# Performance work log

Hardware: AMD Instinct MI355X
Metric: run time of the kernel (lower is better)

The kernel has to match this reference:

```python
import jax, jax.numpy as jnp
import numpy as np

TAU_MEM = 20.0          # tau for both ExpLeak (syn) and LIF (mem)
SPIKE_THRESHOLD = 1.0
WIDTH_GRAD = 0.5        # surrogate gradient width (unused in fwd)
SCALE_GRAD = 1.0


def setup_inputs() -> dict:
    key = jax.random.key(0)
    k1, k2 = jax.random.split(key)
    x = jax.random.normal(k1, (32, 2048, 512, 1), dtype=jnp.float32)
    weight = jax.random.uniform(k2, (1, 1), dtype=jnp.float32)  # Linear(1,1,bias=False) weight (set to scalar `weight` in torch)
    return {"x": x, "weight": weight}


def reference(x, weight):
    # x: (B, T, N, 1); weight: (1, 1)
    alpha = jnp.exp(jnp.asarray(-1.0 / TAU_MEM, dtype=x.dtype))
    i_in = x * weight[0, 0]                      # Linear(1,1,no bias)
    i_in = jnp.moveaxis(i_in, 1, 0)              # (T, B, N, 1) for scan over time

    def step(carry, i_t):
        v_syn, v_mem = carry
        # ExpLeak, norm_input=False: v_syn = alpha*v_syn + input
        v_syn = alpha * v_syn + i_t
        # LIF, norm_input=False: decay then integrate synaptic current
        v_mem = alpha * v_mem + v_syn
        # SingleSpike: at most one spike per step
        spk = (v_mem >= SPIKE_THRESHOLD).astype(v_mem.dtype)
        # MembraneSubtract reset
        v_mem = v_mem - SPIKE_THRESHOLD * spk
        return (v_syn, v_mem), spk

    zeros = jnp.zeros_like(i_in[0])
    _, spikes = jax.lax.scan(step, (zeros, zeros), i_in)
    return jnp.moveaxis(spikes, 0, 1)            # (B, T, N, 1)
```

## Files before the change

### kernel.cpp

```cpp
#include <hip/hip_runtime.h>
#include <math.h>


constexpr int T_ = 2048;
constexpr int N_ = 512;
constexpr int TILE = 64;
constexpr int NTILE = T_ / TILE;
constexpr int NCH = 64;
constexpr int NBUF = 4;

typedef const __attribute__((address_space(1))) void* gas_ptr;
typedef __attribute__((address_space(3))) void* las_ptr;

__global__ __launch_bounds__(192, 1)
void exodus_tri_kernel(const float* __restrict__ x,
                       const float* __restrict__ wptr,
                       float* __restrict__ out) {
    __shared__ float XBUF[NBUF][TILE][NCH];
    __shared__ float SBUF[2][TILE][NCH];

    const int blk  = blockIdx.x;
    const int b    = blk >> 3;
    const int n0   = (blk & 7) * NCH;
    const int wave = threadIdx.x >> 6;
    const int lane = threadIdx.x & 63;

    if (wave == 1) {
        const int plane = lane >> 4;
        const int sub   = lane & 15;
        const float* __restrict__ gl =
            x + (size_t)b * T_ * N_ + (size_t)plane * N_ + n0 + sub * 4;

#define ISSUE_TILE(TT)                                                        \
        {                                                                     \
            const float* __restrict__ g_ =                                    \
                gl + (size_t)(TT) * TILE * N_;                                \
            _Pragma("unroll")                                                 \
            for (int j0_ = 0; j0_ < TILE; j0_ += 4) {                         \
                __builtin_amdgcn_global_load_lds(                             \
                    (gas_ptr)(g_ + (size_t)j0_ * N_),                         \
                    (las_ptr)&XBUF[(TT) & (NBUF - 1)][j0_][0], 16, 0, 0);     \
            }                                                                 \
        }

        ISSUE_TILE(0);
        ISSUE_TILE(1);
        __builtin_amdgcn_sched_barrier(0);
        asm volatile("s_waitcnt vmcnt(16)");
        __builtin_amdgcn_sched_barrier(0);
        __builtin_amdgcn_s_barrier();

        for (int t = 0; t < NTILE; ++t) {
            if (t + 2 < NTILE) {
                ISSUE_TILE(t + 2);
                __builtin_amdgcn_sched_barrier(0);
                asm volatile("s_waitcnt vmcnt(16)");
            } else {
                asm volatile("s_waitcnt vmcnt(0)");
            }
            __builtin_amdgcn_sched_barrier(0);
            __builtin_amdgcn_s_barrier();
        }
#undef ISSUE_TILE
    } else if (wave == 0) {
        const float w = wptr[0];
        const float alpha = (float)exp((double)(-1.0f / 20.0f));
        float vsyn = 0.0f, vmem = 0.0f;

        __builtin_amdgcn_s_barrier();

        for (int t = 0; t < NTILE; ++t) {
            const int xb = t & (NBUF - 1);
            const int sb = t & 1;
            __builtin_amdgcn_sched_barrier(0);

            float xv[TILE];
#pragma unroll
            for (int j = 0; j < TILE; ++j) xv[j] = XBUF[xb][j][lane];

#pragma unroll
            for (int j = 0; j < TILE; ++j) {
                const float i_t = __fmul_rn(xv[j], w);
                vsyn = __fadd_rn(__fmul_rn(alpha, vsyn), i_t);
                const float va = __fadd_rn(__fmul_rn(alpha, vmem), vsyn);
                const bool fire = (va >= 1.0f);
                SBUF[sb][j][lane] = fire ? 1.0f : 0.0f;
                vmem = fire ? __fsub_rn(va, 1.0f) : va;
            }
            __builtin_amdgcn_sched_barrier(0);
            asm volatile("s_waitcnt lgkmcnt(0)");
            __builtin_amdgcn_sched_barrier(0);
            __builtin_amdgcn_s_barrier();
        }
    } else {
        const int plane = lane >> 4;
        const int sub   = lane & 15;
        float* __restrict__ ow =
            out + (size_t)b * T_ * N_ + (size_t)plane * N_ + n0 + sub * 4;

        __builtin_amdgcn_s_barrier();

        for (int t = 0; t < NTILE; ++t) {
            if (t >= 1) {
                const int sb = (t - 1) & 1;
                float4 v[16];
#pragma unroll
                for (int k = 0; k < 16; ++k)
                    v[k] = *(const float4*)&SBUF[sb][4 * k + plane][sub * 4];
                float* __restrict__ o = ow + (size_t)(t - 1) * TILE * N_;
#pragma unroll
                for (int k = 0; k < 16; ++k)
                    *(float4*)(o + (size_t)(4 * k) * N_) = v[k];
            }
            __builtin_amdgcn_sched_barrier(0);
            asm volatile("s_waitcnt lgkmcnt(0)");
            __builtin_amdgcn_sched_barrier(0);
            __builtin_amdgcn_s_barrier();
        }
        {
            const int sb = (NTILE - 1) & 1;
            float4 v[16];
#pragma unroll
            for (int k = 0; k < 16; ++k)
                v[k] = *(const float4*)&SBUF[sb][4 * k + plane][sub * 4];
            float* __restrict__ o = ow + (size_t)(NTILE - 1) * TILE * N_;
#pragma unroll
            for (int k = 0; k < 16; ++k)
                *(float4*)(o + (size_t)(4 * k) * N_) = v[k];
        }
    }
}

extern "C" void kernel_launch(void* const* d_in, const int* in_sizes, int n_in,
                              void* d_out, int out_size, void* d_ws, size_t ws_size,
                              hipStream_t stream) {
    const float* x = (const float*)d_in[0];
    const float* w = (const float*)d_in[1];
    float* out = (float*)d_out;

    dim3 grid(256);
    dim3 block(192);
    hipLaunchKernelGGL(exodus_tri_kernel, grid, block, 0, stream, x, w, out);
}
```

Baseline: 245.9 us.

## Widen blocks to 256-column rows with four compute waves and smaller tiles

Each block now covers 256 contiguous neurons of one batch, so every tile row is a contiguous 1KB load or store. Four compute waves run the recurrence in parallel, with one dedicated loader wave and one dedicated store wave. The time tile shrinks from 64 to 16 steps and prefetch depth grows to three tiles. The grid drops from 256 to 64 blocks, which may leave most CUs idle and cap memory bandwidth, and the per-tile barrier count rises fourfold.

```diff
diff --git a/kernel.cpp b/kernel.cpp
--- a/kernel.cpp
+++ b/kernel.cpp
@@ -4,57 +4,57 @@
 
 constexpr int T_ = 2048;
 constexpr int N_ = 512;
-constexpr int TILE = 64;
+constexpr int NSPAN = 256;
+constexpr int TILE = 16;
 constexpr int NTILE = T_ / TILE;
-constexpr int NCH = 64;
 constexpr int NBUF = 4;
 
 typedef const __attribute__((address_space(1))) void* gas_ptr;
 typedef __attribute__((address_space(3))) void* las_ptr;
 
-__global__ __launch_bounds__(192, 1)
-void exodus_tri_kernel(const float* __restrict__ x,
+__global__ __launch_bounds__(384, 1)
+void exodus_row_kernel(const float* __restrict__ x,
                        const float* __restrict__ wptr,
                        float* __restrict__ out) {
-    __shared__ float XBUF[NBUF][TILE][NCH];
-    __shared__ float SBUF[2][TILE][NCH];
+    __shared__ __align__(16) float XBUF[NBUF][TILE][NSPAN];
+    __shared__ __align__(16) float SBUF[2][TILE][NSPAN];
 
     const int blk  = blockIdx.x;
-    const int b    = blk >> 3;
-    const int n0   = (blk & 7) * NCH;
+    const int b    = blk & 31;
+    const int h    = blk >> 5;
     const int wave = threadIdx.x >> 6;
     const int lane = threadIdx.x & 63;
 
-    if (wave == 1) {
-        const int plane = lane >> 4;
-        const int sub   = lane & 15;
-        const float* __restrict__ gl =
-            x + (size_t)b * T_ * N_ + (size_t)plane * N_ + n0 + sub * 4;
+    const size_t rowbase = (size_t)b * T_ * N_ + (size_t)h * NSPAN;
+
+    if (wave == 4) {
+        const float* __restrict__ gl = x + rowbase + (size_t)lane * 4;
 
 #define ISSUE_TILE(TT)                                                        \
         {                                                                     \
             const float* __restrict__ g_ =                                    \
                 gl + (size_t)(TT) * TILE * N_;                                \
             _Pragma("unroll")                                                 \
-            for (int j0_ = 0; j0_ < TILE; j0_ += 4) {                         \
+            for (int j_ = 0; j_ < TILE; ++j_) {                               \
                 __builtin_amdgcn_global_load_lds(                             \
-                    (gas_ptr)(g_ + (size_t)j0_ * N_),                         \
-                    (las_ptr)&XBUF[(TT) & (NBUF - 1)][j0_][0], 16, 0, 0);     \
+                    (gas_ptr)(g_ + (size_t)j_ * N_),                          \
+                    (las_ptr)&XBUF[(TT) & (NBUF - 1)][j_][0], 16, 0, 0);      \
             }                                                                 \
         }
 
         ISSUE_TILE(0);
         ISSUE_TILE(1);
+        ISSUE_TILE(2);
         __builtin_amdgcn_sched_barrier(0);
-        asm volatile("s_waitcnt vmcnt(16)");
+        asm volatile("s_waitcnt vmcnt(32)");
         __builtin_amdgcn_sched_barrier(0);
         __builtin_amdgcn_s_barrier();
 
         for (int t = 0; t < NTILE; ++t) {
-            if (t + 2 < NTILE) {
-                ISSUE_TILE(t + 2);
+            if (t + 3 < NTILE) {
+                ISSUE_TILE(t + 3);
                 __builtin_amdgcn_sched_barrier(0);
-                asm volatile("s_waitcnt vmcnt(16)");
+                asm volatile("s_waitcnt vmcnt(32)");
             } else {
                 asm volatile("s_waitcnt vmcnt(0)");
             }
@@ -62,7 +62,41 @@
             __builtin_amdgcn_s_barrier();
         }
 #undef ISSUE_TILE
-    } else if (wave == 0) {
+    } else if (wave == 5) {
+        float* __restrict__ ow = out + rowbase + (size_t)lane * 4;
+
+        __builtin_amdgcn_s_barrier();
+
+        for (int t = 0; t < NTILE; ++t) {
+            if (t >= 1) {
+                const int sb = (t - 1) & 1;
+                float4 v[TILE];
+#pragma unroll
+                for (int j = 0; j < TILE; ++j)
+                    v[j] = *(const float4*)&SBUF[sb][j][lane * 4];
+                float* __restrict__ o = ow + (size_t)(t - 1) * TILE * N_;
+#pragma unroll
+                for (int j = 0; j < TILE; ++j)
+                    *(float4*)(o + (size_t)j * N_) = v[j];
+            }
+            __builtin_amdgcn_sched_barrier(0);
+            asm volatile("s_waitcnt lgkmcnt(0)");
+            __builtin_amdgcn_sched_barrier(0);
+            __builtin_amdgcn_s_barrier();
+        }
+        {
+            const int sb = (NTILE - 1) & 1;
+            float4 v[TILE];
+#pragma unroll
+            for (int j = 0; j < TILE; ++j)
+                v[j] = *(const float4*)&SBUF[sb][j][lane * 4];
+            float* __restrict__ o = ow + (size_t)(NTILE - 1) * TILE * N_;
+#pragma unroll
+            for (int j = 0; j < TILE; ++j)
+                *(float4*)(o + (size_t)j * N_) = v[j];
+        }
+    } else {
+        const int col = wave * 64 + lane;
         const float w = wptr[0];
         const float alpha = (float)exp((double)(-1.0f / 20.0f));
         float vsyn = 0.0f, vmem = 0.0f;
@@ -76,7 +110,7 @@
 
             float xv[TILE];
 #pragma unroll
-            for (int j = 0; j < TILE; ++j) xv[j] = XBUF[xb][j][lane];
+            for (int j = 0; j < TILE; ++j) xv[j] = XBUF[xb][j][col];
 
 #pragma unroll
             for (int j = 0; j < TILE; ++j) {
@@ -84,49 +118,13 @@
                 vsyn = __fadd_rn(__fmul_rn(alpha, vsyn), i_t);
                 const float va = __fadd_rn(__fmul_rn(alpha, vmem), vsyn);
                 const bool fire = (va >= 1.0f);
-                SBUF[sb][j][lane] = fire ? 1.0f : 0.0f;
+                SBUF[sb][j][col] = fire ? 1.0f : 0.0f;
                 vmem = fire ? __fsub_rn(va, 1.0f) : va;
             }
             __builtin_amdgcn_sched_barrier(0);
             asm volatile("s_waitcnt lgkmcnt(0)");
             __builtin_amdgcn_sched_barrier(0);
             __builtin_amdgcn_s_barrier();
-        }
-    } else {
-        const int plane = lane >> 4;
-        const int sub   = lane & 15;
-        float* __restrict__ ow =
-            out + (size_t)b * T_ * N_ + (size_t)plane * N_ + n0 + sub * 4;
-
-        __builtin_amdgcn_s_barrier();
-
-        for (int t = 0; t < NTILE; ++t) {
-            if (t >= 1) {
-                const int sb = (t - 1) & 1;
-                float4 v[16];
-#pragma unroll
-                for (int k = 0; k < 16; ++k)
-                    v[k] = *(const float4*)&SBUF[sb][4 * k + plane][sub * 4];
-                float* __restrict__ o = ow + (size_t)(t - 1) * TILE * N_;
-#pragma unroll
-                for (int k = 0; k < 16; ++k)
-                    *(float4*)(o + (size_t)(4 * k) * N_) = v[k];
-            }
-            __builtin_amdgcn_sched_barrier(0);
-            asm volatile("s_waitcnt lgkmcnt(0)");
-            __builtin_amdgcn_sched_barrier(0);
-            __builtin_amdgcn_s_barrier();
-        }
-        {
-            const int sb = (NTILE - 1) & 1;
-            float4 v[16];
-#pragma unroll
-            for (int k = 0; k < 16; ++k)
-                v[k] = *(const float4*)&SBUF[sb][4 * k + plane][sub * 4];
-            float* __restrict__ o = ow + (size_t)(NTILE - 1) * TILE * N_;
-#pragma unroll
-            for (int k = 0; k < 16; ++k)
-                *(float4*)(o + (size_t)(4 * k) * N_) = v[k];
         }
     }
 }
@@ -138,7 +136,7 @@
     const float* w = (const float*)d_in[1];
     float* out = (float*)d_out;
 
-    dim3 grid(256);
-    dim3 block(192);
-    hipLaunchKernelGGL(exodus_tri_kernel, grid, block, 0, stream, x, w, out);
+    dim3 grid(64);
+    dim3 block(384);
+    hipLaunchKernelGGL(exodus_row_kernel, grid, block, 0, stream, x, w, out);
 }
```

Result: slower. 290.5 us (+18.2%).

## Spread tile loads over four producer waves and stores over two writer waves

Applied to the files above, without the earlier changes.

The single loader wave becomes four loader waves that take turns issuing tiles, with 7 tiles of prefetch depth into an 8-slot buffer. The single store wave becomes two writer waves that alternate tiles. The tile size is halved to 32 so the scan wave syncs at a finer grain. The aim is to raise memory-level parallelism so the serial scan wave is not stalled waiting on loads or buffer reuse. In exchange there are twice as many block barriers per run and more complex buffer-index bookkeeping.

```diff
diff --git a/kernel.cpp b/kernel.cpp
--- a/kernel.cpp
+++ b/kernel.cpp
@@ -4,20 +4,23 @@
 
 constexpr int T_ = 2048;
 constexpr int N_ = 512;
-constexpr int TILE = 64;
+constexpr int TILE = 32;
 constexpr int NTILE = T_ / TILE;
 constexpr int NCH = 64;
-constexpr int NBUF = 4;
+constexpr int NXB = 8;
+constexpr int NSB = 4;
 
 typedef const __attribute__((address_space(1))) void* gas_ptr;
 typedef __attribute__((address_space(3))) void* las_ptr;
 
-__global__ __launch_bounds__(192, 1)
-void exodus_tri_kernel(const float* __restrict__ x,
-                       const float* __restrict__ wptr,
-                       float* __restrict__ out) {
-    __shared__ float XBUF[NBUF][TILE][NCH];
-    __shared__ float SBUF[2][TILE][NCH];
+#define SB() __builtin_amdgcn_sched_barrier(0)
+
+__global__ __launch_bounds__(448, 1)
+void exodus_ms_kernel(const float* __restrict__ x,
+                      const float* __restrict__ wptr,
+                      float* __restrict__ out) {
+    __shared__ __align__(16) float XBUF[NXB][TILE][NCH];
+    __shared__ __align__(16) float SBUF[NSB][TILE][NCH];
 
     const int blk  = blockIdx.x;
     const int b    = blk >> 3;
@@ -25,7 +28,8 @@
     const int wave = threadIdx.x >> 6;
     const int lane = threadIdx.x & 63;
 
-    if (wave == 1) {
+    if (wave >= 1 && wave <= 4) {
+        const int p = wave - 1;
         const int plane = lane >> 4;
         const int sub   = lane & 15;
         const float* __restrict__ gl =
@@ -36,43 +40,85 @@
             const float* __restrict__ g_ =                                    \
                 gl + (size_t)(TT) * TILE * N_;                                \
             _Pragma("unroll")                                                 \
-            for (int j0_ = 0; j0_ < TILE; j0_ += 4) {                         \
+            for (int r_ = 0; r_ < TILE; r_ += 4) {                            \
                 __builtin_amdgcn_global_load_lds(                             \
-                    (gas_ptr)(g_ + (size_t)j0_ * N_),                         \
-                    (las_ptr)&XBUF[(TT) & (NBUF - 1)][j0_][0], 16, 0, 0);     \
+                    (gas_ptr)(g_ + (size_t)r_ * N_),                          \
+                    (las_ptr)&XBUF[(TT) & (NXB - 1)][r_][0], 16, 0, 0);       \
             }                                                                 \
         }
 
-        ISSUE_TILE(0);
-        ISSUE_TILE(1);
-        __builtin_amdgcn_sched_barrier(0);
-        asm volatile("s_waitcnt vmcnt(16)");
-        __builtin_amdgcn_sched_barrier(0);
+        ISSUE_TILE(p);
+        ISSUE_TILE(p + 4);
+        SB();
+        asm volatile("s_waitcnt vmcnt(8)");
+        SB();
         __builtin_amdgcn_s_barrier();
 
-        for (int t = 0; t < NTILE; ++t) {
-            if (t + 2 < NTILE) {
-                ISSUE_TILE(t + 2);
-                __builtin_amdgcn_sched_barrier(0);
-                asm volatile("s_waitcnt vmcnt(16)");
-            } else {
-                asm volatile("s_waitcnt vmcnt(0)");
+        for (int k = 0; k < NTILE; ++k) {
+            if ((k & 3) == ((p + 1) & 3)) {
+                if (k + 7 < NTILE) {
+                    ISSUE_TILE(k + 7);
+                    SB();
+                    asm volatile("s_waitcnt vmcnt(8)");
+                } else {
+                    SB();
+                    asm volatile("s_waitcnt vmcnt(0)");
+                }
+                SB();
             }
-            __builtin_amdgcn_sched_barrier(0);
             __builtin_amdgcn_s_barrier();
         }
 #undef ISSUE_TILE
-    } else if (wave == 0) {
+    } else if (wave >= 5) {
+        const int wbit = wave - 5;
+        const int plane = lane >> 4;
+        const int sub   = lane & 15;
+        float* __restrict__ ow =
+            out + (size_t)b * T_ * N_ + (size_t)plane * N_ + n0 + sub * 4;
+
+        __builtin_amdgcn_s_barrier();
+
+        for (int k = 0; k < NTILE; ++k) {
+            if (k >= 1 && ((k - 1) & 1) == wbit) {
+                const int j = k - 1;
+                const int sb = j & (NSB - 1);
+                float4 v[TILE / 4];
+#pragma unroll
+                for (int g = 0; g < TILE / 4; ++g)
+                    v[g] = *(const float4*)&SBUF[sb][4 * g + plane][sub * 4];
+                float* __restrict__ o = ow + (size_t)j * TILE * N_;
+#pragma unroll
+                for (int g = 0; g < TILE / 4; ++g)
+                    *(float4*)(o + (size_t)(4 * g) * N_) = v[g];
+                SB();
+                asm volatile("s_waitcnt lgkmcnt(0)");
+                SB();
+            }
+            __builtin_amdgcn_s_barrier();
+        }
+        if (wbit == ((NTILE - 1) & 1)) {
+            const int j = NTILE - 1;
+            const int sb = j & (NSB - 1);
+            float4 v[TILE / 4];
+#pragma unroll
+            for (int g = 0; g < TILE / 4; ++g)
+                v[g] = *(const float4*)&SBUF[sb][4 * g + plane][sub * 4];
+            float* __restrict__ o = ow + (size_t)j * TILE * N_;
+#pragma unroll
+            for (int g = 0; g < TILE / 4; ++g)
+                *(float4*)(o + (size_t)(4 * g) * N_) = v[g];
+        }
+    } else {
         const float w = wptr[0];
         const float alpha = (float)exp((double)(-1.0f / 20.0f));
         float vsyn = 0.0f, vmem = 0.0f;
 
         __builtin_amdgcn_s_barrier();
 
-        for (int t = 0; t < NTILE; ++t) {
-            const int xb = t & (NBUF - 1);
-            const int sb = t & 1;
-            __builtin_amdgcn_sched_barrier(0);
+        for (int k = 0; k < NTILE; ++k) {
+            const int xb = k & (NXB - 1);
+            const int sb = k & (NSB - 1);
+            SB();
 
             float xv[TILE];
 #pragma unroll
@@ -87,46 +133,10 @@
                 SBUF[sb][j][lane] = fire ? 1.0f : 0.0f;
                 vmem = fire ? __fsub_rn(va, 1.0f) : va;
             }
-            __builtin_amdgcn_sched_barrier(0);
+            SB();
             asm volatile("s_waitcnt lgkmcnt(0)");
-            __builtin_amdgcn_sched_barrier(0);
+            SB();
             __builtin_amdgcn_s_barrier();
-        }
-    } else {
-        const int plane = lane >> 4;
-        const int sub   = lane & 15;
-        float* __restrict__ ow =
-            out + (size_t)b * T_ * N_ + (size_t)plane * N_ + n0 + sub * 4;
-
-        __builtin_amdgcn_s_barrier();
-
-        for (int t = 0; t < NTILE; ++t) {
-            if (t >= 1) {
-                const int sb = (t - 1) & 1;
-                float4 v[16];
-#pragma unroll
-                for (int k = 0; k < 16; ++k)
-                    v[k] = *(const float4*)&SBUF[sb][4 * k + plane][sub * 4];
-                float* __restrict__ o = ow + (size_t)(t - 1) * TILE * N_;
-#pragma unroll
-                for (int k = 0; k < 16; ++k)
-                    *(float4*)(o + (size_t)(4 * k) * N_) = v[k];
-            }
-            __builtin_amdgcn_sched_barrier(0);
-            asm volatile("s_waitcnt lgkmcnt(0)");
-            __builtin_amdgcn_sched_barrier(0);
-            __builtin_amdgcn_s_barrier();
-        }
-        {
-            const int sb = (NTILE - 1) & 1;
-            float4 v[16];
-#pragma unroll
-            for (int k = 0; k < 16; ++k)
-                v[k] = *(const float4*)&SBUF[sb][4 * k + plane][sub * 4];
-            float* __restrict__ o = ow + (size_t)(NTILE - 1) * TILE * N_;
-#pragma unroll
-            for (int k = 0; k < 16; ++k)
-                *(float4*)(o + (size_t)(4 * k) * N_) = v[k];
         }
     }
 }
@@ -139,6 +149,6 @@
     float* out = (float*)d_out;
 
     dim3 grid(256);
-    dim3 block(192);
-    hipLaunchKernelGGL(exodus_tri_kernel, grid, block, 0, stream, x, w, out);
+    dim3 block(448);
+    hipLaunchKernelGGL(exodus_ms_kernel, grid, block, 0, stream, x, w, out);
 }
```

New measurement: 246.0 us. No clear change (+0.0%).
